# Performance work log

Measured on AMD Instinct MI355X. Metric: run time of the kernel, lower is better.

Reference implementation:

```python
import jax, jax.numpy as jnp
import numpy as np

# Static graph-batch configuration (equal-size graphs so per-graph top-k is static)
B = 256          # number of graphs in the batch
N = 400          # nodes per graph
D = 256          # in_dim
DEG = 32         # average degree
E = B * N * DEG  # total edges
RATIO = 0.5
K = int(np.ceil(RATIO * N))  # nodes kept per graph by mytopk
NT = B * N


def setup_inputs() -> dict:
    key = jax.random.key(0)
    k1, k2, k3, k4 = jax.random.split(key, 4)
    feature = jax.random.normal(k1, (NT, D), dtype=jnp.float32)
    W = jax.random.normal(k2, (D, 1), dtype=jnp.float32) * (1.0 / np.sqrt(D))
    b = jnp.zeros((1,), dtype=jnp.float32)
    # edges stay within each graph: global id = graph_offset + local id
    g = jnp.repeat(jnp.arange(B, dtype=jnp.int32), N * DEG)  # [E] graph id per edge
    src = g * N + jax.random.randint(k3, (E,), 0, N, dtype=jnp.int32)
    dst = g * N + jax.random.randint(k4, (E,), 0, N, dtype=jnp.int32)
    return {"feature": feature, "W": W, "b": b, "src": src, "dst": dst}


def _forward(feature, W, b, src, dst):
    # --- GraphConv(in_dim, 1), norm='both' (dgl): h = D_in^-1/2 A D_out^-1/2 (X W) + b
    ones_e = jnp.ones((E,), dtype=feature.dtype)
    deg_out = jax.ops.segment_sum(ones_e, src, num_segments=NT)
    deg_in = jax.ops.segment_sum(ones_e, dst, num_segments=NT)
    norm_out = jnp.maximum(deg_out, 1.0) ** -0.5  # dgl clamps degree to min 1
    norm_in = jnp.maximum(deg_in, 1.0) ** -0.5
    h = (feature @ W) * norm_out[:, None]                      # [NT,1]
    agg = jax.ops.segment_sum(h[src], dst, num_segments=NT)    # [NT,1]
    score = (agg * norm_in[:, None] + b)[:, 0]                 # [NT]

    # --- mytopk: per-graph top-k node selection by score (descending)
    score2d = score.reshape(B, N)
    _, idx = jax.lax.top_k(score2d, K)                         # [B,K] local ids
    offsets = (jnp.arange(B, dtype=jnp.int32) * N)[:, None]
    perm = (idx.astype(jnp.int32) + offsets).reshape(-1)       # [B*K] global ids

    # complement nodes (mask trick in the original): ascending order per graph
    sel = jnp.zeros((NT,), dtype=bool).at[perm].set(True)
    sel2d = sel.reshape(B, N).astype(jnp.int32)
    order = jnp.argsort(sel2d, axis=1, stable=True)[:, : N - K]  # unselected first
    perm_com = (order.astype(jnp.int32) + offsets).reshape(-1)   # [B*(N-K)]

    # --- gated feature gathers
    feature_dis = feature[perm] * jnp.tanh(score[perm])[:, None]
    feature_com = feature[perm_com] * jnp.tanh(score[perm_com])[:, None]

    # --- subgraph structure as static-shape edge masks (dgl.node_subgraph keeps
    #     edges whose both endpoints are selected)
    e_dis_mask = sel[src] & sel[dst]
    e_com_mask = (~sel[src]) & (~sel[dst])

    score_soft = jax.nn.softmax(score, axis=0)  # Softmax(dim=0) over all nodes
    return feature_dis, feature_com, perm, perm_com, score_soft, e_dis_mask, e_com_mask


def reference(feature, W, b, src, dst):
    return _forward(feature, W, b, src, dst)
```

## Files before the change

### kernel.cpp

```cpp
#include <hip/hip_runtime.h>
#include <math.h>

#define B_    256
#define N_    400
#define D_    256
#define EPG_  12800
#define E_    3276800
#define NT_   102400
#define K_    200
#define NKC_  200

#define O_FDIS 0
#define O_FCOM 13107200
#define O_PERM 26214400
#define O_PCOM 26265600
#define O_SOFT 26316800
#define O_EDIS 26419200
#define O_ECOM 29696000

#define NEG_INF (-3.402823466e38f)

__global__ __launch_bounds__(256) void k_h(const float* __restrict__ feat,
                                           const float* __restrict__ W,
                                           float* __restrict__ hraw) {
    const int gw   = (blockIdx.x * 256 + threadIdx.x) >> 6;
    const int lane = threadIdx.x & 63;
    const float4 w4 = ((const float4*)W)[lane];
    const int r0 = gw * 4;
    const float4* fb = (const float4*)feat;
    float4 a0 = fb[(size_t)(r0    ) * 64 + lane];
    float4 a1 = fb[(size_t)(r0 + 1) * 64 + lane];
    float4 a2 = fb[(size_t)(r0 + 2) * 64 + lane];
    float4 a3 = fb[(size_t)(r0 + 3) * 64 + lane];
    float d0 = a0.x*w4.x + a0.y*w4.y + a0.z*w4.z + a0.w*w4.w;
    float d1 = a1.x*w4.x + a1.y*w4.y + a1.z*w4.z + a1.w*w4.w;
    float d2 = a2.x*w4.x + a2.y*w4.y + a2.z*w4.z + a2.w*w4.w;
    float d3 = a3.x*w4.x + a3.y*w4.y + a3.z*w4.z + a3.w*w4.w;
    #pragma unroll
    for (int off = 32; off > 0; off >>= 1) {
        d0 += __shfl_down(d0, off, 64);
        d1 += __shfl_down(d1, off, 64);
        d2 += __shfl_down(d2, off, 64);
        d3 += __shfl_down(d3, off, 64);
    }
    if (lane == 0) {
        hraw[r0    ] = d0;
        hraw[r0 + 1] = d1;
        hraw[r0 + 2] = d2;
        hraw[r0 + 3] = d3;
    }
}

__global__ __launch_bounds__(1024) void k_fused(const int* __restrict__ src,
                                                const int* __restrict__ dst,
                                                const float* __restrict__ hraw,
                                                const float* __restrict__ bp,
                                                float* __restrict__ score,
                                                float* __restrict__ pm,
                                                float* __restrict__ ps,
                                                int* __restrict__ orow,
                                                float* __restrict__ out) {
    __shared__ float hl[N_], scl[N_];
    __shared__ int   ho[N_], hi[N_], smask[N_];
    const int g = blockIdx.x, tid = threadIdx.x;
    const int nbase = g * N_, ebase = g * EPG_;
    const int wave = tid >> 6, lane = tid & 63;

    float hr = 0.0f;
    if (tid < N_) hr = hraw[nbase + tid];

    if (tid < N_) { ho[tid] = 0; hi[tid] = 0; scl[tid] = 0.0f; }
    __syncthreads();

    const int4* s4 = (const int4*)(src + ebase);
    const int4* d4 = (const int4*)(dst + ebase);
    for (int i = tid; i < EPG_ / 4; i += 1024) {
        int4 s = s4[i]; int4 d = d4[i];
        atomicAdd(&ho[s.x - nbase], 1);
        atomicAdd(&ho[s.y - nbase], 1);
        atomicAdd(&ho[s.z - nbase], 1);
        atomicAdd(&ho[s.w - nbase], 1);
        atomicAdd(&hi[d.x - nbase], 1);
        atomicAdd(&hi[d.y - nbase], 1);
        atomicAdd(&hi[d.z - nbase], 1);
        atomicAdd(&hi[d.w - nbase], 1);
    }
    __syncthreads();

    if (tid < N_)
        hl[tid] = hr * (1.0f / sqrtf(fmaxf((float)ho[tid], 1.0f)));
    __syncthreads();

    for (int i = tid; i < EPG_ / 4; i += 1024) {
        int4 s = s4[i]; int4 d = d4[i];
        atomicAdd(&scl[d.x - nbase], hl[s.x - nbase]);
        atomicAdd(&scl[d.y - nbase], hl[s.y - nbase]);
        atomicAdd(&scl[d.z - nbase], hl[s.z - nbase]);
        atomicAdd(&scl[d.w - nbase], hl[s.w - nbase]);
    }
    __syncthreads();

    const float bb = bp[0];
    if (tid < N_) {
        float v = scl[tid] * (1.0f / sqrtf(fmaxf((float)hi[tid], 1.0f))) + bb;
        scl[tid] = v;
        score[nbase + tid] = v;
    }
    __syncthreads();

    if (tid < N_) {
        const float v = scl[tid];
        int r = 0;
        for (int j = 0; j < N_; ++j) {
            float u = scl[j];
            r += (u > v) || (u == v && j < tid);
        }
        const int selb = (r < K_) ? 1 : 0;
        smask[tid] = selb;
        if (selb) {
            orow[nbase + tid] = g * K_ + r;
            out[O_PERM + g * K_ + r] = (float)(nbase + tid);
        }
    }
    if (wave == 15) {
        float m = NEG_INF;
        for (int i = lane; i < N_; i += 64) m = fmaxf(m, scl[i]);
        #pragma unroll
        for (int o = 32; o > 0; o >>= 1) m = fmaxf(m, __shfl_xor(m, o, 64));
        float s = 0.0f;
        for (int i = lane; i < N_; i += 64) s += expf(scl[i] - m);
        #pragma unroll
        for (int o = 32; o > 0; o >>= 1) s += __shfl_xor(s, o, 64);
        if (lane == 0) { pm[g] = m; ps[g] = s; }
    }
    __syncthreads();

    if (tid < N_ && !smask[tid]) {
        int pos = 0;
        for (int u = 0; u < tid; ++u) pos += (smask[u] == 0);
        orow[nbase + tid] = B_ * K_ + g * NKC_ + pos;
        out[O_PCOM + g * NKC_ + pos] = (float)(nbase + tid);
    }

    float4* mdis = (float4*)(out + O_EDIS) + g * (EPG_ / 4);
    float4* mcom = (float4*)(out + O_ECOM) + g * (EPG_ / 4);
    for (int i = tid; i < EPG_ / 4; i += 1024) {
        int4 s = s4[i]; int4 d = d4[i];
        int a0 = smask[s.x - nbase], a1 = smask[s.y - nbase];
        int a2 = smask[s.z - nbase], a3 = smask[s.w - nbase];
        int b0 = smask[d.x - nbase], b1 = smask[d.y - nbase];
        int b2 = smask[d.z - nbase], b3 = smask[d.w - nbase];
        float4 vdis, vcom;
        vdis.x = (a0 & b0) ? 1.0f : 0.0f;  vcom.x = (a0 | b0) ? 0.0f : 1.0f;
        vdis.y = (a1 & b1) ? 1.0f : 0.0f;  vcom.y = (a1 | b1) ? 0.0f : 1.0f;
        vdis.z = (a2 & b2) ? 1.0f : 0.0f;  vcom.z = (a2 | b2) ? 0.0f : 1.0f;
        vdis.w = (a3 & b3) ? 1.0f : 0.0f;  vcom.w = (a3 | b3) ? 0.0f : 1.0f;
        mdis[i] = vdis;
        mcom[i] = vcom;
    }
}

__global__ __launch_bounds__(256) void k_soft_comb(const float* pm, const float* ps, float* red2) {
    __shared__ float rm[256], rs[256];
    int tid = threadIdx.x;
    float m = pm[tid];
    rm[tid] = m; __syncthreads();
    for (int o = 128; o > 0; o >>= 1) { if (tid < o) rm[tid] = fmaxf(rm[tid], rm[tid + o]); __syncthreads(); }
    float M = rm[0]; __syncthreads();
    rs[tid] = ps[tid] * expf(m - M); __syncthreads();
    for (int o = 128; o > 0; o >>= 1) { if (tid < o) rs[tid] += rs[tid + o]; __syncthreads(); }
    if (tid == 0) { red2[0] = M; red2[1] = rs[0]; }
}

__global__ __launch_bounds__(256) void k_gather(const float* __restrict__ feat,
                                                const float* __restrict__ score,
                                                const int* __restrict__ orow,
                                                const float* __restrict__ red2,
                                                float* __restrict__ out) {
    const int gw   = (blockIdx.x * 256 + threadIdx.x) >> 6;
    const int lane = threadIdx.x & 63;
    const int n0 = gw * 4;
    const float4* fb = (const float4*)feat;
    float4 v0 = fb[(size_t)(n0    ) * 64 + lane];
    float4 v1 = fb[(size_t)(n0 + 1) * 64 + lane];
    float4 v2 = fb[(size_t)(n0 + 2) * 64 + lane];
    float4 v3 = fb[(size_t)(n0 + 3) * 64 + lane];
    float s0 = score[n0], s1 = score[n0 + 1], s2 = score[n0 + 2], s3 = score[n0 + 3];
    int   r0 = orow[n0],  r1 = orow[n0 + 1],  r2 = orow[n0 + 2],  r3 = orow[n0 + 3];
    float t0 = tanhf(s0), t1 = tanhf(s1), t2 = tanhf(s2), t3 = tanhf(s3);
    v0.x *= t0; v0.y *= t0; v0.z *= t0; v0.w *= t0;
    v1.x *= t1; v1.y *= t1; v1.z *= t1; v1.w *= t1;
    v2.x *= t2; v2.y *= t2; v2.z *= t2; v2.w *= t2;
    v3.x *= t3; v3.y *= t3; v3.z *= t3; v3.w *= t3;
    ((float4*)(out + (size_t)r0 * D_))[lane] = v0;
    ((float4*)(out + (size_t)r1 * D_))[lane] = v1;
    ((float4*)(out + (size_t)r2 * D_))[lane] = v2;
    ((float4*)(out + (size_t)r3 * D_))[lane] = v3;
    if (lane == 0) {
        float M = red2[0], S = red2[1];
        out[O_SOFT + n0    ] = expf(s0 - M) / S;
        out[O_SOFT + n0 + 1] = expf(s1 - M) / S;
        out[O_SOFT + n0 + 2] = expf(s2 - M) / S;
        out[O_SOFT + n0 + 3] = expf(s3 - M) / S;
    }
}

extern "C" void kernel_launch(void* const* d_in, const int* in_sizes, int n_in,
                              void* d_out, int out_size, void* d_ws, size_t ws_size,
                              hipStream_t stream) {
    const float* feat = (const float*)d_in[0];
    const float* W    = (const float*)d_in[1];
    const float* bp   = (const float*)d_in[2];
    const int*   src  = (const int*)d_in[3];
    const int*   dst  = (const int*)d_in[4];
    float* out = (float*)d_out;

    char* ws = (char*)d_ws;
    float* hraw  = (float*)(ws + 0);
    float* score = (float*)(ws + 409600);
    int*   orow  = (int*)  (ws + 819200);
    float* pm    = (float*)(ws + 1228800);
    float* ps    = (float*)(ws + 1229824);
    float* red2  = (float*)(ws + 1230848);

    k_h        <<<NT_ / 16, 256, 0, stream>>>(feat, W, hraw);
    k_fused    <<<B_,      1024, 0, stream>>>(src, dst, hraw, bp,
                                              score, pm, ps, orow, out);
    k_soft_comb<<<1,        256, 0, stream>>>(pm, ps, red2);
    k_gather   <<<NT_ / 16, 256, 0, stream>>>(feat, score, orow, red2, out);
}
```

Measured before the change: 286.8 us.

## Fuse feature-weight dot product into per-graph kernel and use nontemporal stores

Removes the separate k_h launch. Each per-graph block now computes its nodes' feature·W dot products with 12 waves while the other 4 waves build the degree histograms concurrently, writing results straight to shared memory. Output stores for the edge masks and gathered features become nontemporal, to avoid polluting cache with write-once data. The trade-off is that only 256 blocks now read the 100 MB feature matrix, and the degree counting runs on a quarter of the block, which may leave the phase bandwidth- or latency-limited.

```diff
diff --git a/kernel.cpp b/kernel.cpp
--- a/kernel.cpp
+++ b/kernel.cpp
@@ -20,40 +20,17 @@
 
 #define NEG_INF (-3.402823466e38f)
 
-__global__ __launch_bounds__(256) void k_h(const float* __restrict__ feat,
-                                           const float* __restrict__ W,
-                                           float* __restrict__ hraw) {
-    const int gw   = (blockIdx.x * 256 + threadIdx.x) >> 6;
-    const int lane = threadIdx.x & 63;
-    const float4 w4 = ((const float4*)W)[lane];
-    const int r0 = gw * 4;
-    const float4* fb = (const float4*)feat;
-    float4 a0 = fb[(size_t)(r0    ) * 64 + lane];
-    float4 a1 = fb[(size_t)(r0 + 1) * 64 + lane];
-    float4 a2 = fb[(size_t)(r0 + 2) * 64 + lane];
-    float4 a3 = fb[(size_t)(r0 + 3) * 64 + lane];
-    float d0 = a0.x*w4.x + a0.y*w4.y + a0.z*w4.z + a0.w*w4.w;
-    float d1 = a1.x*w4.x + a1.y*w4.y + a1.z*w4.z + a1.w*w4.w;
-    float d2 = a2.x*w4.x + a2.y*w4.y + a2.z*w4.z + a2.w*w4.w;
-    float d3 = a3.x*w4.x + a3.y*w4.y + a3.z*w4.z + a3.w*w4.w;
-    #pragma unroll
-    for (int off = 32; off > 0; off >>= 1) {
-        d0 += __shfl_down(d0, off, 64);
-        d1 += __shfl_down(d1, off, 64);
-        d2 += __shfl_down(d2, off, 64);
-        d3 += __shfl_down(d3, off, 64);
-    }
-    if (lane == 0) {
-        hraw[r0    ] = d0;
-        hraw[r0 + 1] = d1;
-        hraw[r0 + 2] = d2;
-        hraw[r0 + 3] = d3;
-    }
-}
-
-__global__ __launch_bounds__(1024) void k_fused(const int* __restrict__ src,
+typedef float nfv4 __attribute__((ext_vector_type(4)));
+
+static __device__ __forceinline__ void nt_store4(float4* p, float4 v) {
+    nfv4 x; x.x = v.x; x.y = v.y; x.z = v.z; x.w = v.w;
+    __builtin_nontemporal_store(x, (nfv4*)p);
+}
+
+__global__ __launch_bounds__(1024) void k_graph(const float* __restrict__ feat,
+                                                const float* __restrict__ W,
+                                                const int* __restrict__ src,
                                                 const int* __restrict__ dst,
-                                                const float* __restrict__ hraw,
                                                 const float* __restrict__ bp,
                                                 float* __restrict__ score,
                                                 float* __restrict__ pm,
@@ -66,29 +43,49 @@
     const int nbase = g * N_, ebase = g * EPG_;
     const int wave = tid >> 6, lane = tid & 63;
 
-    float hr = 0.0f;
-    if (tid < N_) hr = hraw[nbase + tid];
-
     if (tid < N_) { ho[tid] = 0; hi[tid] = 0; scl[tid] = 0.0f; }
     __syncthreads();
 
     const int4* s4 = (const int4*)(src + ebase);
     const int4* d4 = (const int4*)(dst + ebase);
-    for (int i = tid; i < EPG_ / 4; i += 1024) {
-        int4 s = s4[i]; int4 d = d4[i];
-        atomicAdd(&ho[s.x - nbase], 1);
-        atomicAdd(&ho[s.y - nbase], 1);
-        atomicAdd(&ho[s.z - nbase], 1);
-        atomicAdd(&ho[s.w - nbase], 1);
-        atomicAdd(&hi[d.x - nbase], 1);
-        atomicAdd(&hi[d.y - nbase], 1);
-        atomicAdd(&hi[d.z - nbase], 1);
-        atomicAdd(&hi[d.w - nbase], 1);
+
+    if (wave < 12) {
+        const float4 w4 = ((const float4*)W)[lane];
+        const float4* fb = (const float4*)feat + (size_t)nbase * 64;
+        for (int r = wave; r < N_; r += 24) {
+            const int r2 = r + 12;
+            float4 a0 = fb[(size_t)r * 64 + lane];
+            float4 a1 = (r2 < N_) ? fb[(size_t)r2 * 64 + lane]
+                                  : make_float4(0.f, 0.f, 0.f, 0.f);
+            float d0 = a0.x*w4.x + a0.y*w4.y + a0.z*w4.z + a0.w*w4.w;
+            float d1 = a1.x*w4.x + a1.y*w4.y + a1.z*w4.z + a1.w*w4.w;
+            #pragma unroll
+            for (int off = 32; off > 0; off >>= 1) {
+                d0 += __shfl_down(d0, off, 64);
+                d1 += __shfl_down(d1, off, 64);
+            }
+            if (lane == 0) {
+                hl[r] = d0;
+                if (r2 < N_) hl[r2] = d1;
+            }
+        }
+    } else {
+        for (int i = tid - 768; i < EPG_ / 4; i += 256) {
+            int4 s = s4[i]; int4 d = d4[i];
+            atomicAdd(&ho[s.x - nbase], 1);
+            atomicAdd(&ho[s.y - nbase], 1);
+            atomicAdd(&ho[s.z - nbase], 1);
+            atomicAdd(&ho[s.w - nbase], 1);
+            atomicAdd(&hi[d.x - nbase], 1);
+            atomicAdd(&hi[d.y - nbase], 1);
+            atomicAdd(&hi[d.z - nbase], 1);
+            atomicAdd(&hi[d.w - nbase], 1);
+        }
     }
     __syncthreads();
 
     if (tid < N_)
-        hl[tid] = hr * (1.0f / sqrtf(fmaxf((float)ho[tid], 1.0f)));
+        hl[tid] = hl[tid] * (1.0f / sqrtf(fmaxf((float)ho[tid], 1.0f)));
     __syncthreads();
 
     for (int i = tid; i < EPG_ / 4; i += 1024) {
@@ -155,8 +152,8 @@
         vdis.y = (a1 & b1) ? 1.0f : 0.0f;  vcom.y = (a1 | b1) ? 0.0f : 1.0f;
         vdis.z = (a2 & b2) ? 1.0f : 0.0f;  vcom.z = (a2 | b2) ? 0.0f : 1.0f;
         vdis.w = (a3 & b3) ? 1.0f : 0.0f;  vcom.w = (a3 | b3) ? 0.0f : 1.0f;
-        mdis[i] = vdis;
-        mcom[i] = vcom;
+        nt_store4(&mdis[i], vdis);
+        nt_store4(&mcom[i], vcom);
     }
 }
 
@@ -192,10 +189,10 @@
     v1.x *= t1; v1.y *= t1; v1.z *= t1; v1.w *= t1;
     v2.x *= t2; v2.y *= t2; v2.z *= t2; v2.w *= t2;
     v3.x *= t3; v3.y *= t3; v3.z *= t3; v3.w *= t3;
-    ((float4*)(out + (size_t)r0 * D_))[lane] = v0;
-    ((float4*)(out + (size_t)r1 * D_))[lane] = v1;
-    ((float4*)(out + (size_t)r2 * D_))[lane] = v2;
-    ((float4*)(out + (size_t)r3 * D_))[lane] = v3;
+    nt_store4(((float4*)(out + (size_t)r0 * D_)) + lane, v0);
+    nt_store4(((float4*)(out + (size_t)r1 * D_)) + lane, v1);
+    nt_store4(((float4*)(out + (size_t)r2 * D_)) + lane, v2);
+    nt_store4(((float4*)(out + (size_t)r3 * D_)) + lane, v3);
     if (lane == 0) {
         float M = red2[0], S = red2[1];
         out[O_SOFT + n0    ] = expf(s0 - M) / S;
@@ -216,15 +213,13 @@
     float* out = (float*)d_out;
 
     char* ws = (char*)d_ws;
-    float* hraw  = (float*)(ws + 0);
-    float* score = (float*)(ws + 409600);
-    int*   orow  = (int*)  (ws + 819200);
-    float* pm    = (float*)(ws + 1228800);
-    float* ps    = (float*)(ws + 1229824);
-    float* red2  = (float*)(ws + 1230848);
-
-    k_h        <<<NT_ / 16, 256, 0, stream>>>(feat, W, hraw);
-    k_fused    <<<B_,      1024, 0, stream>>>(src, dst, hraw, bp,
+    float* score = (float*)(ws + 0);
+    int*   orow  = (int*)  (ws + 409600);
+    float* pm    = (float*)(ws + 819200);
+    float* ps    = (float*)(ws + 820224);
+    float* red2  = (float*)(ws + 821248);
+
+    k_graph    <<<B_,      1024, 0, stream>>>(feat, W, src, dst, bp,
                                               score, pm, ps, orow, out);
     k_soft_comb<<<1,        256, 0, stream>>>(pm, ps, red2);
     k_gather   <<<NT_ / 16, 256, 0, stream>>>(feat, score, orow, red2, out);
```

Result: no change. 285.7 us (-0.4%).

## Split edge-mask writing into grid-wide kernel, shuffle-based ranking, ballot prefix for complement

Applied to the files above, without the earlier changes.

Moves the per-edge subgraph mask output out of the 256-block graph kernel into a separate kernel launched over all edges. That kernel reads a global selection array and writes with nontemporal stores, so the large mask write is no longer confined to 256 workgroups. The top-k rank loop now reads candidate scores through wave shuffles from registers instead of LDS. The complement position is computed from ballot masks and popcounts instead of a serial scan. The feature gather also uses nontemporal stores. The cost is an extra launch, a global selection buffer, and gathers of that buffer from global memory instead of LDS.

```diff
diff --git a/kernel.cpp b/kernel.cpp
--- a/kernel.cpp
+++ b/kernel.cpp
@@ -19,6 +19,13 @@
 #define O_ECOM 29696000
 
 #define NEG_INF (-3.402823466e38f)
+
+typedef float nfv4 __attribute__((ext_vector_type(4)));
+
+static __device__ __forceinline__ void nt_store4(float4* p, float4 v) {
+    nfv4 x; x.x = v.x; x.y = v.y; x.z = v.z; x.w = v.w;
+    __builtin_nontemporal_store(x, (nfv4*)p);
+}
 
 __global__ __launch_bounds__(256) void k_h(const float* __restrict__ feat,
                                            const float* __restrict__ W,
@@ -51,17 +58,20 @@
     }
 }
 
-__global__ __launch_bounds__(1024) void k_fused(const int* __restrict__ src,
+__global__ __launch_bounds__(1024) void k_graph(const int* __restrict__ src,
                                                 const int* __restrict__ dst,
                                                 const float* __restrict__ hraw,
                                                 const float* __restrict__ bp,
                                                 float* __restrict__ score,
                                                 float* __restrict__ pm,
                                                 float* __restrict__ ps,
+                                                int* __restrict__ sel,
                                                 int* __restrict__ orow,
                                                 float* __restrict__ out) {
     __shared__ float hl[N_], scl[N_];
-    __shared__ int   ho[N_], hi[N_], smask[N_];
+    __shared__ int   ho[N_], hi[N_];
+    __shared__ unsigned long long bmask[7];
+
     const int g = blockIdx.x, tid = threadIdx.x;
     const int nbase = g * N_, ebase = g * EPG_;
     const int wave = tid >> 6, lane = tid & 63;
@@ -74,6 +84,7 @@
 
     const int4* s4 = (const int4*)(src + ebase);
     const int4* d4 = (const int4*)(dst + ebase);
+
     for (int i = tid; i < EPG_ / 4; i += 1024) {
         int4 s = s4[i]; int4 d = d4[i];
         atomicAdd(&ho[s.x - nbase], 1);
@@ -108,19 +119,33 @@
     }
     __syncthreads();
 
-    if (tid < N_) {
-        const float v = scl[tid];
-        int r = 0;
-        for (int j = 0; j < N_; ++j) {
-            float u = scl[j];
-            r += (u > v) || (u == v && j < tid);
+    bool selb = false;
+    if (tid < 448) {
+        float sreg[7];
+        #pragma unroll
+        for (int t = 0; t < 7; ++t) {
+            const int j = t * 64 + lane;
+            sreg[t] = (j < N_) ? scl[j] : NEG_INF;
         }
-        const int selb = (r < K_) ? 1 : 0;
-        smask[tid] = selb;
+        const float v = (tid < N_) ? scl[tid] : NEG_INF;
+        int rnk = 0;
+        #pragma unroll
+        for (int t = 0; t < 7; ++t) {
+            #pragma unroll
+            for (int l2 = 0; l2 < 64; ++l2) {
+                const float u = __shfl(sreg[t], l2, 64);
+                const int j = t * 64 + l2;
+                rnk += ((u > v) || (u == v && j < tid)) ? 1 : 0;
+            }
+        }
+        selb = (tid < N_) && (rnk < K_);
+        if (tid < N_) sel[nbase + tid] = selb ? 1 : 0;
         if (selb) {
-            orow[nbase + tid] = g * K_ + r;
-            out[O_PERM + g * K_ + r] = (float)(nbase + tid);
+            orow[nbase + tid] = g * K_ + rnk;
+            out[O_PERM + g * K_ + rnk] = (float)(nbase + tid);
         }
+        unsigned long long bal = __ballot(selb);
+        if (lane == 0) bmask[wave] = bal;
     }
     if (wave == 15) {
         float m = NEG_INF;
@@ -135,28 +160,15 @@
     }
     __syncthreads();
 
-    if (tid < N_ && !smask[tid]) {
-        int pos = 0;
-        for (int u = 0; u < tid; ++u) pos += (smask[u] == 0);
+    if (tid < N_ && !selb) {
+        int nsel = 0;
+        #pragma unroll
+        for (int w = 0; w < 7; ++w)
+            if (w < wave) nsel += (int)__popcll(bmask[w]);
+        nsel += (int)__popcll(bmask[wave] & ((1ull << lane) - 1ull));
+        const int pos = tid - nsel;
         orow[nbase + tid] = B_ * K_ + g * NKC_ + pos;
         out[O_PCOM + g * NKC_ + pos] = (float)(nbase + tid);
-    }
-
-    float4* mdis = (float4*)(out + O_EDIS) + g * (EPG_ / 4);
-    float4* mcom = (float4*)(out + O_ECOM) + g * (EPG_ / 4);
-    for (int i = tid; i < EPG_ / 4; i += 1024) {
-        int4 s = s4[i]; int4 d = d4[i];
-        int a0 = smask[s.x - nbase], a1 = smask[s.y - nbase];
-        int a2 = smask[s.z - nbase], a3 = smask[s.w - nbase];
-        int b0 = smask[d.x - nbase], b1 = smask[d.y - nbase];
-        int b2 = smask[d.z - nbase], b3 = smask[d.w - nbase];
-        float4 vdis, vcom;
-        vdis.x = (a0 & b0) ? 1.0f : 0.0f;  vcom.x = (a0 | b0) ? 0.0f : 1.0f;
-        vdis.y = (a1 & b1) ? 1.0f : 0.0f;  vcom.y = (a1 | b1) ? 0.0f : 1.0f;
-        vdis.z = (a2 & b2) ? 1.0f : 0.0f;  vcom.z = (a2 | b2) ? 0.0f : 1.0f;
-        vdis.w = (a3 & b3) ? 1.0f : 0.0f;  vcom.w = (a3 | b3) ? 0.0f : 1.0f;
-        mdis[i] = vdis;
-        mcom[i] = vcom;
     }
 }
 
@@ -170,6 +182,24 @@
     rs[tid] = ps[tid] * expf(m - M); __syncthreads();
     for (int o = 128; o > 0; o >>= 1) { if (tid < o) rs[tid] += rs[tid + o]; __syncthreads(); }
     if (tid == 0) { red2[0] = M; red2[1] = rs[0]; }
+}
+
+__global__ __launch_bounds__(256) void k_mask(const int* __restrict__ src,
+                                              const int* __restrict__ dst,
+                                              const int* __restrict__ sel,
+                                              float* __restrict__ out) {
+    const int i = blockIdx.x * 256 + threadIdx.x;
+    int4 s = ((const int4*)src)[i];
+    int4 d = ((const int4*)dst)[i];
+    int a0 = sel[s.x], a1 = sel[s.y], a2 = sel[s.z], a3 = sel[s.w];
+    int b0 = sel[d.x], b1 = sel[d.y], b2 = sel[d.z], b3 = sel[d.w];
+    float4 mdis, mcom;
+    mdis.x = (a0 & b0) ? 1.0f : 0.0f;  mcom.x = (a0 | b0) ? 0.0f : 1.0f;
+    mdis.y = (a1 & b1) ? 1.0f : 0.0f;  mcom.y = (a1 | b1) ? 0.0f : 1.0f;
+    mdis.z = (a2 & b2) ? 1.0f : 0.0f;  mcom.z = (a2 | b2) ? 0.0f : 1.0f;
+    mdis.w = (a3 & b3) ? 1.0f : 0.0f;  mcom.w = (a3 | b3) ? 0.0f : 1.0f;
+    nt_store4(((float4*)(out + O_EDIS)) + i, mdis);
+    nt_store4(((float4*)(out + O_ECOM)) + i, mcom);
 }
 
 __global__ __launch_bounds__(256) void k_gather(const float* __restrict__ feat,
@@ -192,10 +222,10 @@
     v1.x *= t1; v1.y *= t1; v1.z *= t1; v1.w *= t1;
     v2.x *= t2; v2.y *= t2; v2.z *= t2; v2.w *= t2;
     v3.x *= t3; v3.y *= t3; v3.z *= t3; v3.w *= t3;
-    ((float4*)(out + (size_t)r0 * D_))[lane] = v0;
-    ((float4*)(out + (size_t)r1 * D_))[lane] = v1;
-    ((float4*)(out + (size_t)r2 * D_))[lane] = v2;
-    ((float4*)(out + (size_t)r3 * D_))[lane] = v3;
+    nt_store4(((float4*)(out + (size_t)r0 * D_)) + lane, v0);
+    nt_store4(((float4*)(out + (size_t)r1 * D_)) + lane, v1);
+    nt_store4(((float4*)(out + (size_t)r2 * D_)) + lane, v2);
+    nt_store4(((float4*)(out + (size_t)r3 * D_)) + lane, v3);
     if (lane == 0) {
         float M = red2[0], S = red2[1];
         out[O_SOFT + n0    ] = expf(s0 - M) / S;
@@ -218,14 +248,16 @@
     char* ws = (char*)d_ws;
     float* hraw  = (float*)(ws + 0);
     float* score = (float*)(ws + 409600);
-    int*   orow  = (int*)  (ws + 819200);
-    float* pm    = (float*)(ws + 1228800);
-    float* ps    = (float*)(ws + 1229824);
-    float* red2  = (float*)(ws + 1230848);
-
-    k_h        <<<NT_ / 16, 256, 0, stream>>>(feat, W, hraw);
-    k_fused    <<<B_,      1024, 0, stream>>>(src, dst, hraw, bp,
-                                              score, pm, ps, orow, out);
-    k_soft_comb<<<1,        256, 0, stream>>>(pm, ps, red2);
-    k_gather   <<<NT_ / 16, 256, 0, stream>>>(feat, score, orow, red2, out);
-}
+    int*   sel   = (int*)  (ws + 819200);
+    int*   orow  = (int*)  (ws + 1228800);
+    float* pm    = (float*)(ws + 1638400);
+    float* ps    = (float*)(ws + 1639424);
+    float* red2  = (float*)(ws + 1640448);
+
+    k_h        <<<NT_ / 16,    256, 0, stream>>>(feat, W, hraw);
+    k_graph    <<<B_,         1024, 0, stream>>>(src, dst, hraw, bp,
+                                                 score, pm, ps, sel, orow, out);
+    k_soft_comb<<<1,           256, 0, stream>>>(pm, ps, red2);
+    k_mask     <<<E_ / 4 / 256, 256, 0, stream>>>(src, dst, sel, out);
+    k_gather   <<<NT_ / 16,    256, 0, stream>>>(feat, score, orow, red2, out);
+}
```

After: 294.0 us. 1.03x slower.
